# Optimization experiments

Measured on AMD Instinct MI355X. Metric: run time of the kernel, lower is better.

The kernel has to match this reference:

```python
import jax, jax.numpy as jnp
import numpy as np

# module config (mirrors init_kwargs)
D_MODEL = 1024
N_HEADS = 16
HEAD_DIM = D_MODEL // N_HEADS
WINDOW = 512
PREFIX = 16
B = 2
S = 4096  # divisible by WINDOW; S > WINDOW + PREFIX -> chunked windowed path


def setup_inputs() -> dict:
    key = jax.random.key(0)
    k1, k2, k3 = jax.random.split(key, 3)
    x = jax.random.normal(k1, (B, S, D_MODEL), dtype=jnp.float32)
    w_qkv = jax.random.normal(k2, (3 * D_MODEL, D_MODEL), dtype=jnp.float32) * 0.02
    w_out = jax.random.normal(k3, (D_MODEL, D_MODEL), dtype=jnp.float32) * 0.02
    return {"x": x, "w_qkv": w_qkv, "w_out": w_out}


def _windowed_global_attention(q, k, v):
    """q,k,v: [B,H,S,Dh]. Causal sliding-window (WINDOW) + global prefix (PREFIX) attention.
    Exactly matches torch's chunked SDPA: for query chunk starting at q_start, allowed keys are
    k_pos < PREFIX (causal) plus local keys in (q_pos-WINDOW, q_pos] with k_pos >= PREFIX."""
    Bb, H, S_, Dh = q.shape
    W, P = WINDOW, PREFIX
    C = S_ // W  # number of query chunks
    scale = 1.0 / np.sqrt(Dh).astype(np.float32)

    qc = q.reshape(Bb, H, C, W, Dh)  # [B,H,C,W,Dh]
    # pad W zero-keys at front so every chunk gathers a uniform 2W-key local tail
    kp = jnp.pad(k, ((0, 0), (0, 0), (W, 0), (0, 0)))
    vp = jnp.pad(v, ((0, 0), (0, 0), (W, 0), (0, 0)))
    tail_idx = jnp.arange(C)[:, None] * W + jnp.arange(2 * W)[None, :]  # [C,2W] (padded coords)
    kt = kp[:, :, tail_idx, :]  # [B,H,C,2W,Dh]
    vt = vp[:, :, tail_idx, :]
    kg = k[:, :, :P, :]  # global prefix keys [B,H,P,Dh]
    vg = v[:, :, :P, :]

    sg = jnp.einsum('bhcqd,bhkd->bhcqk', qc, kg) * scale   # [B,H,C,W,P]
    st = jnp.einsum('bhcqd,bhckd->bhcqk', qc, kt) * scale  # [B,H,C,W,2W]

    q_pos = jnp.arange(C)[:, None] * W + jnp.arange(W)[None, :]          # [C,W]
    kt_pos = jnp.arange(C)[:, None] * W - W + jnp.arange(2 * W)[None, :]  # [C,2W]
    # global prefix: causal only
    mg = jnp.arange(P)[None, None, :] <= q_pos[:, :, None]                # [C,W,P]
    # local tail: causal & within window & not already covered by global prefix (and not padding)
    diff = q_pos[:, :, None] - kt_pos[:, None, :]                          # [C,W,2W]
    mt = (diff >= 0) & (diff < W) & (kt_pos[:, None, :] >= P)

    neg = jnp.asarray(-1e9, sg.dtype)
    scores = jnp.concatenate([
        jnp.where(mg[None, None], sg, neg),
        jnp.where(mt[None, None], st, neg),
    ], axis=-1)  # [B,H,C,W,P+2W]
    attn = jax.nn.softmax(scores, axis=-1)

    vcat = jnp.concatenate([
        jnp.broadcast_to(vg[:, :, None], (Bb, H, C, P, Dh)), vt
    ], axis=3)  # [B,H,C,P+2W,Dh]
    out = jnp.einsum('bhcqk,bhckd->bhcqd', attn, vcat)
    return out.reshape(Bb, H, S_, Dh)


def reference(x, w_qkv, w_out):
    Bb, S_, Dm = x.shape
    qkv = x @ w_qkv.T                      # [B,S,3*Dm]
    q, k, v = jnp.split(qkv, 3, axis=-1)
    def heads(t):
        return t.reshape(Bb, S_, N_HEADS, HEAD_DIM).transpose(0, 2, 1, 3)
    q, k, v = heads(q), heads(k), heads(v)  # [B,H,S,Dh]
    o = _windowed_global_attention(q, k, v)
    o = o.transpose(0, 2, 1, 3).reshape(Bb, S_, Dm)
    return o @ w_out.T
```

## Files before the change

### kernel.cpp

```cpp
#include <hip/hip_runtime.h>
#include <hip/hip_bf16.h>

#define AS1 __attribute__((address_space(1)))
#define AS3 __attribute__((address_space(3)))

typedef unsigned short u16;
typedef short bf16x8 __attribute__((ext_vector_type(8)));
typedef unsigned short u16x8 __attribute__((ext_vector_type(8)));
typedef float f32x4 __attribute__((ext_vector_type(4)));

#define MFMA16 __builtin_amdgcn_mfma_f32_16x16x32_bf16


__device__ __forceinline__ u16 f2bf(float f) {
  union { float f; unsigned u; } c; c.f = f;
  unsigned u = c.u;
  u = u + 0x7fffu + ((u >> 16) & 1u);
  return (u16)(u >> 16);
}

__device__ __forceinline__ float fexp2(float x) {
#if __has_builtin(__builtin_amdgcn_exp2f)
  return __builtin_amdgcn_exp2f(x);
#else
  return exp2f(x);
#endif
}

__device__ __forceinline__ unsigned pack_bf(float a, float b) {
  union { float f; unsigned u; } ua, ub; ua.f = a; ub.f = b;
  return __builtin_amdgcn_perm(ub.u, ua.u, 0x07060302u);
}

__device__ __forceinline__ void gl_lds16(const void* g, void* l) {
  __builtin_amdgcn_global_load_lds((const AS1 void*)g, (AS3 void*)l, 16, 0, 0);
}


__global__ void cast_all_kernel(const float* __restrict__ x,
                                const float* __restrict__ wqkv,
                                const float* __restrict__ wout,
                                u16* __restrict__ ws) {
  int i = blockIdx.x * blockDim.x + threadIdx.x;
  const float4* src;
  int rel;
  size_t matbase;
  if (i < 2097152)      { src = (const float4*)x + i;                rel = i;           matbase = 0; }
  else if (i < 2883584) { src = (const float4*)wqkv + (i - 2097152); rel = i - 2097152; matbase = 8388608; }
  else                  { src = (const float4*)wout + (i - 2883584); rel = i - 2883584; matbase = 11534336; }
  float4 f = *src;
  ushort4 o;
  o.x = f2bf(f.x); o.y = f2bf(f.y); o.z = f2bf(f.z); o.w = f2bf(f.w);
  int fe  = rel * 4;
  int row = fe >> 10, c = fe & 1023;
  int newc = (c & ~63) | (((((c >> 3) ^ row) & 7) << 3)) | (c & 7);
  ((ushort4*)ws)[(matbase + (size_t)row * 1024 + newc) >> 2] = o;
}


template<int EPI>
__global__ __launch_bounds__(256) void gemm_bt(
    const u16* __restrict__ A, const u16* __restrict__ Bm,
    float* __restrict__ Cf,
    u16* __restrict__ qd, u16* __restrict__ kd, u16* __restrict__ vd,
    int M, int N, int K)
{
  __shared__ u16 As[128 * 64];
  __shared__ u16 Bs[128 * 64];

  const int tid  = threadIdx.x;
  const int wave = tid >> 6, lane = tid & 63;
  const int quad = lane >> 4, l16 = lane & 15;
  const int bm = blockIdx.y * 128, bn = blockIdx.x * 128;
  const int wm = (wave >> 1) * 64, wn = (wave & 1) * 64;

  f32x4 acc[4][4] = {};

  const int srow = wave * 32 + (lane >> 3);
  const int scol = (lane & 7) * 8;

  for (int kt = 0; kt < K; kt += 64) {
    __syncthreads();
    #pragma unroll
    for (int i = 0; i < 4; ++i) {
      gl_lds16(&A[(size_t)(bm + srow + i * 8) * K + kt + scol], &As[(wave * 32 + i * 8) * 64]);
      gl_lds16(&Bm[(size_t)(bn + srow + i * 8) * K + kt + scol], &Bs[(wave * 32 + i * 8) * 64]);
    }
    __syncthreads();
    #pragma unroll
    for (int kk = 0; kk < 64; kk += 32) {
      bf16x8 af[4], bb[4];
      #pragma unroll
      for (int i = 0; i < 4; ++i) {
        int row = wm + i * 16 + l16;
        af[i] = *(const bf16x8*)&As[row * 64 + (((((kk >> 3) + quad) ^ row) & 7) << 3)];
      }
      #pragma unroll
      for (int j = 0; j < 4; ++j) {
        int row = wn + j * 16 + l16;
        bb[j] = *(const bf16x8*)&Bs[row * 64 + (((((kk >> 3) + quad) ^ row) & 7) << 3)];
      }
      #pragma unroll
      for (int i = 0; i < 4; ++i)
        #pragma unroll
        for (int j = 0; j < 4; ++j)
          acc[i][j] = MFMA16(af[i], bb[j], acc[i][j], 0, 0, 0);
    }
  }

  #pragma unroll
  for (int i = 0; i < 4; ++i) {
    #pragma unroll
    for (int j = 0; j < 4; ++j) {
      #pragma unroll
      for (int r = 0; r < 4; ++r) {
        int m = bm + wm + i * 16 + quad * 4 + r;
        int n = bn + wn + j * 16 + l16;
        float val = acc[i][j][r];
        if (EPI == 0) {
          Cf[(size_t)m * N + n] = val;
        } else {
          int part = n >> 10, rem = n & 1023;
          int h = rem >> 6, d = rem & 63;
          int b = m >> 12, s = m & 4095;
          if (part == 0) val *= 0.1803368801111244f;
          u16* dst = (part == 0) ? qd : (part == 1) ? kd : vd;
          dst[((size_t)((b * 16 + h) * 4096 + s)) * 64 + d] = f2bf(val);
        }
      }
    }
  }
}


__global__ __launch_bounds__(256) void pack_v(const u16* __restrict__ vb,
                                              u16* __restrict__ vt) {
  __shared__ u16 Lt[64 * 72];
  const int tid = threadIdx.x, bid = blockIdx.x;
  const int bh = bid & 31, t = bid >> 5;
  const size_t base = (size_t)bh << 18;
  #pragma unroll
  for (int c = 0; c < 2; ++c) {
    int idx = tid * 8 + c * 2048;
    int row = idx >> 6, col = idx & 63;
    u16x8 vv = *(const u16x8*)&vb[base + (size_t)(t * 64 + row) * 64 + col];
    #pragma unroll
    for (int s = 0; s < 8; ++s) Lt[(col + s) * 72 + row] = vv[s];
  }
  __syncthreads();
  #pragma unroll
  for (int c = 0; c < 2; ++c) {
    int w = tid + c * 256;
    int dh = w >> 3, k8 = w & 7;
    u16x8 o;
    #pragma unroll
    for (int s = 0; s < 8; ++s) o[s] = Lt[dh * 72 + k8 * 8 + s];
    int off = ((dh >> 4) << 10) | ((k8 >> 2) << 9) | ((k8 & 3) << 7) | ((dh & 15) << 3);
    *(u16x8*)&vt[base + (size_t)t * 4096 + off] = o;
  }
}


__global__ __launch_bounds__(256) void attn_kernel(
    const u16* __restrict__ qb, const u16* __restrict__ kb,
    const u16* __restrict__ vt, u16* __restrict__ ob)
{
  __shared__ u16 Ps[4][32 * 64];

  const int tid  = threadIdx.x;
  const int wave = tid >> 6;
  const int lane = tid & 63;
  const int quad = lane >> 4, l16 = lane & 15;
  const int bid  = blockIdx.x;
  const int bh   = bid & 31;
  const int t0   = (((bid >> 5) << 2) | wave) << 5;
  const size_t base = (size_t)bh << 18;
  u16* __restrict__ ps = &Ps[wave][0];

  const int l64 = l16 * 64 + quad * 8;
  const u16* vbase = vt + base + lane * 8;

  const u16* qp = qb + base + (size_t)t0 * 64 + l64;
  bf16x8 bq00 = *(const bf16x8*)(qp);
  bf16x8 bq01 = *(const bf16x8*)(qp + 32);
  bf16x8 bq10 = *(const bf16x8*)(qp + 1024);
  bf16x8 bq11 = *(const bf16x8*)(qp + 1056);

  f32x4 oacc[2][4] = {};
  f32x4 lacc[2] = {};
  bf16x8 ones;
  #pragma unroll
  for (int s = 0; s < 8; ++s) ones[s] = (short)0x3F80;

  const int lo = max(0, t0 - 511) >> 6;
  const int hi = (t0 + 31) >> 6;

  auto loadK = [&](int kb0, bf16x8 (&kf)[4][2]) {
    #pragma unroll
    for (int j = 0; j < 4; ++j) {
      const u16* krow = kb + base + (size_t)(kb0 + j * 16) * 64 + l64;
      kf[j][0] = *(const bf16x8*)(krow);
      kf[j][1] = *(const bf16x8*)(krow + 32);
    }
  };

  bf16x8 ka[4][2], kb2[4][2];

  {
    const u16* kpre = kb + base + l64;
    bf16x8 pk0 = *(const bf16x8*)(kpre);
    bf16x8 pk1 = *(const bf16x8*)(kpre + 32);
    loadK(lo << 6, ka);
    bf16x8 pv[4];
    #pragma unroll
    for (int jd = 0; jd < 4; ++jd)
      pv[jd] = *(const bf16x8*)(vbase + jd * 1024);

    #pragma unroll
    for (int i = 0; i < 2; ++i) {
      f32x4 t4 = {};
      t4 = MFMA16(pk0, i ? bq10 : bq00, t4, 0, 0, 0);
      t4 = MFMA16(pk1, i ? bq11 : bq01, t4, 0, 0, 0);
      int row = i * 16 + l16;
      int qpos = t0 + row;
      float p[4];
      #pragma unroll
      for (int r = 0; r < 4; ++r) {
        int kpos = quad * 4 + r;
        p[r] = (kpos <= qpos) ? fexp2(t4[r]) : 0.f;
      }
      uint2 w;
      w.x = pack_bf(p[0], p[1]);
      w.y = pack_bf(p[2], p[3]);
      *(uint2*)&ps[row * 64 + ((quad ^ l16) & 15) * 4] = w;
      uint2 z; z.x = 0u; z.y = 0u;
      *(uint2*)&ps[row * 64 + (((4 + quad) ^ l16) & 15) * 4] = z;
    }
    #pragma unroll
    for (int i = 0; i < 2; ++i) {
      int row = i * 16 + l16;
      uint2 r0 = *(uint2*)&ps[row * 64 + (((2 * quad) ^ l16) & 15) * 4];
      uint2 r1 = *(uint2*)&ps[row * 64 + (((2 * quad + 1) ^ l16) & 15) * 4];
      union { uint4 u; bf16x8 v; } cc; cc.u = make_uint4(r0.x, r0.y, r1.x, r1.y);
      bf16x8 ap = cc.v;
      lacc[i] = MFMA16(ap, ones, lacc[i], 0, 0, 0);
      #pragma unroll
      for (int jd = 0; jd < 4; ++jd)
        oacc[i][jd] = MFMA16(ap, pv[jd], oacc[i][jd], 0, 0, 0);
    }
  }

  auto tilec = [&](int kb0, bf16x8 (&kf)[4][2]) {
    #pragma unroll
    for (int j = 0; j < 4; ++j) {
      const int kmin = kb0 + j * 16;
      #pragma unroll
      for (int i = 0; i < 2; ++i) {
        const int qmin = t0 + i * 16;
        const int row  = i * 16 + l16;
        uint2* dst = (uint2*)&ps[row * 64 + (((j * 4 + quad) ^ l16) & 15) * 4];
        const bool sub_masked = (kmin > qmin + 15) || (qmin - kmin >= 527) || (kmin < 16);
        if (sub_masked) { uint2 z; z.x = 0u; z.y = 0u; *dst = z; continue; }
        f32x4 t4 = {};
        t4 = MFMA16(kf[j][0], i ? bq10 : bq00, t4, 0, 0, 0);
        t4 = MFMA16(kf[j][1], i ? bq11 : bq01, t4, 0, 0, 0);
        const bool sub_ok = (kmin + 15 <= qmin) && (qmin + 15 - kmin < 512);
        float p[4];
        if (sub_ok) {
          #pragma unroll
          for (int r = 0; r < 4; ++r) p[r] = fexp2(t4[r]);
        } else {
          int qpos = t0 + row;
          #pragma unroll
          for (int r = 0; r < 4; ++r) {
            int kpos = kmin + quad * 4 + r;
            unsigned diff = (unsigned)(qpos - kpos);
            p[r] = (diff < 512u) ? fexp2(t4[r]) : 0.f;
          }
        }
        uint2 w;
        w.x = pack_bf(p[0], p[1]);
        w.y = pack_bf(p[2], p[3]);
        *dst = w;
      }
    }
    const u16* vp = vbase + (size_t)kb0 * 64;
    #pragma unroll
    for (int h = 0; h < 2; ++h) {
      bf16x8 bv0 = *(const bf16x8*)(vp + h * 512);
      bf16x8 bv1 = *(const bf16x8*)(vp + 1024 + h * 512);
      bf16x8 bv2 = *(const bf16x8*)(vp + 2048 + h * 512);
      bf16x8 bv3 = *(const bf16x8*)(vp + 3072 + h * 512);
      #pragma unroll
      for (int i = 0; i < 2; ++i) {
        int row = i * 16 + l16;
        int g0 = h * 8 + 2 * quad;
        uint2 r0 = *(uint2*)&ps[row * 64 + ((g0 ^ l16) & 15) * 4];
        uint2 r1 = *(uint2*)&ps[row * 64 + (((g0 + 1) ^ l16) & 15) * 4];
        union { uint4 u; bf16x8 v; } cc; cc.u = make_uint4(r0.x, r0.y, r1.x, r1.y);
        bf16x8 ap = cc.v;
        lacc[i] = MFMA16(ap, ones, lacc[i], 0, 0, 0);
        oacc[i][0] = MFMA16(ap, bv0, oacc[i][0], 0, 0, 0);
        oacc[i][1] = MFMA16(ap, bv1, oacc[i][1], 0, 0, 0);
        oacc[i][2] = MFMA16(ap, bv2, oacc[i][2], 0, 0, 0);
        oacc[i][3] = MFMA16(ap, bv3, oacc[i][3], 0, 0, 0);
      }
    }
  };

  for (int t = lo; t <= hi; t += 2) {
    if (t + 1 <= hi) loadK((t + 1) << 6, kb2);
    tilec(t << 6, ka);
    if (t + 1 <= hi) {
      if (t + 2 <= hi) loadK((t + 2) << 6, ka);
      tilec((t + 1) << 6, kb2);
    }
  }

  const int b = bh >> 4, h = bh & 15;
  #pragma unroll
  for (int i = 0; i < 2; ++i) {
    #pragma unroll
    for (int r = 0; r < 4; ++r) {
      float inv = 1.f / lacc[i][r];
      int srow = t0 + i * 16 + quad * 4 + r;
      size_t rowoff = ((size_t)(b * 4096 + srow)) * 1024 + h * 64;
      #pragma unroll
      for (int jd = 0; jd < 4; ++jd) {
        int g = ((jd * 2 + (l16 >> 3)) ^ srow) & 7;
        ob[rowoff + (g << 3) + (l16 & 7)] = f2bf(oacc[i][jd][r] * inv);
      }
    }
  }
}


extern "C" void kernel_launch(void* const* d_in, const int* in_sizes, int n_in,
                              void* d_out, int out_size, void* d_ws, size_t ws_size,
                              hipStream_t stream) {
  const float* x    = (const float*)d_in[0];
  const float* wqkv = (const float*)d_in[1];
  const float* wout = (const float*)d_in[2];
  float* out = (float*)d_out;

  u16* ws    = (u16*)d_ws;
  u16* xb    = ws;
  u16* wqkvb = xb + (size_t)8192 * 1024;
  u16* woutb = wqkvb + (size_t)3072 * 1024;
  u16* qbuf  = woutb + (size_t)1024 * 1024;
  u16* kbuf  = qbuf + (size_t)8388608;
  u16* vbuf  = kbuf + (size_t)8388608;
  u16* vtb   = vbuf + (size_t)8388608;
  u16* obuf  = xb;

  cast_all_kernel<<<12288, 256, 0, stream>>>(x, wqkv, wout, ws);

  gemm_bt<1><<<dim3(24, 64), 256, 0, stream>>>(xb, wqkvb, nullptr, qbuf, kbuf, vbuf,
                                               8192, 3072, 1024);
  pack_v<<<2048, 256, 0, stream>>>(vbuf, vtb);
  attn_kernel<<<1024, 256, 0, stream>>>(qbuf, kbuf, vtb, obuf);
  gemm_bt<0><<<dim3(8, 64), 256, 0, stream>>>(obuf, woutb, out, nullptr, nullptr, nullptr,
                                              8192, 1024, 1024);
}
```

Measured before the change: 241.4 us.

## Rewrite GEMM with 256x128 tiles, double-buffered LDS, and interleaved MFMA scheduling

```diff
diff --git a/kernel.cpp b/kernel.cpp
--- a/kernel.cpp
+++ b/kernel.cpp
@@ -10,6 +10,10 @@
 typedef float f32x4 __attribute__((ext_vector_type(4)));
 
 #define MFMA16 __builtin_amdgcn_mfma_f32_16x16x32_bf16
+
+#define SBAR()  asm volatile("s_barrier" ::: "memory")
+#define WAITV(N) asm volatile("s_waitcnt vmcnt(" #N ")" ::: "memory")
+#define WAITL0() asm volatile("s_waitcnt lgkmcnt(0)" ::: "memory")
 
 
 __device__ __forceinline__ u16 f2bf(float f) {
@@ -59,73 +63,148 @@
 
 
 template<int EPI>
-__global__ __launch_bounds__(256) void gemm_bt(
+__global__ __launch_bounds__(512, 2) void gemm_bt2(
     const u16* __restrict__ A, const u16* __restrict__ Bm,
     float* __restrict__ Cf,
     u16* __restrict__ qd, u16* __restrict__ kd, u16* __restrict__ vd,
     int M, int N, int K)
 {
-  __shared__ u16 As[128 * 64];
-  __shared__ u16 Bs[128 * 64];
+  __shared__ u16 As[2][2][128 * 64];
+  __shared__ u16 Bs[2][128 * 64];
 
   const int tid  = threadIdx.x;
   const int wave = tid >> 6, lane = tid & 63;
   const int quad = lane >> 4, l16 = lane & 15;
-  const int bm = blockIdx.y * 128, bn = blockIdx.x * 128;
-  const int wm = (wave >> 1) * 64, wn = (wave & 1) * 64;
-
-  f32x4 acc[4][4] = {};
-
-  const int srow = wave * 32 + (lane >> 3);
-  const int scol = (lane & 7) * 8;
-
-  for (int kt = 0; kt < K; kt += 64) {
-    __syncthreads();
-    #pragma unroll
-    for (int i = 0; i < 4; ++i) {
-      gl_lds16(&A[(size_t)(bm + srow + i * 8) * K + kt + scol], &As[(wave * 32 + i * 8) * 64]);
-      gl_lds16(&Bm[(size_t)(bn + srow + i * 8) * K + kt + scol], &Bs[(wave * 32 + i * 8) * 64]);
-    }
-    __syncthreads();
-    #pragma unroll
-    for (int kk = 0; kk < 64; kk += 32) {
-      bf16x8 af[4], bb[4];
-      #pragma unroll
-      for (int i = 0; i < 4; ++i) {
-        int row = wm + i * 16 + l16;
-        af[i] = *(const bf16x8*)&As[row * 64 + (((((kk >> 3) + quad) ^ row) & 7) << 3)];
-      }
-      #pragma unroll
-      for (int j = 0; j < 4; ++j) {
-        int row = wn + j * 16 + l16;
-        bb[j] = *(const bf16x8*)&Bs[row * 64 + (((((kk >> 3) + quad) ^ row) & 7) << 3)];
-      }
-      #pragma unroll
-      for (int i = 0; i < 4; ++i)
-        #pragma unroll
-        for (int j = 0; j < 4; ++j)
-          acc[i][j] = MFMA16(af[i], bb[j], acc[i][j], 0, 0, 0);
-    }
-  }
-
-  #pragma unroll
-  for (int i = 0; i < 4; ++i) {
-    #pragma unroll
-    for (int j = 0; j < 4; ++j) {
+
+  const int gx  = gridDim.x;
+  const int nwg = gx * gridDim.y;
+  const int lin = blockIdx.y * gx + blockIdx.x;
+  const int q8  = nwg >> 3;
+  const int swz = (lin & 7) * q8 + (lin >> 3);
+  const int bm = (swz / gx) * 256;
+  const int bn = (swz % gx) * 128;
+
+  const int hA = wave >> 2;
+  const int wn = (wave & 3) * 32;
+
+  const int srow = tid >> 3;
+  const int scol = (tid & 7) * 8;
+  const u16* Ab = A  + (size_t)(bm + srow) * K + scol;
+  const u16* Bb = Bm + (size_t)(bn + srow) * K + scol;
+  const int ldsw = wave * 512;
+
+  const int NT = K >> 6;
+
+  auto stA = [&](int t, int h) {
+    int d = t & 1;
+    #pragma unroll
+    for (int i = 0; i < 2; ++i)
+      gl_lds16(Ab + (size_t)(128 * h + 64 * i) * K + t * 64,
+               &As[d][h][ldsw + i * 4096]);
+  };
+  auto stB = [&](int t) {
+    int d = t & 1;
+    #pragma unroll
+    for (int i = 0; i < 2; ++i)
+      gl_lds16(Bb + (size_t)(64 * i) * K + t * 64,
+               &Bs[d][ldsw + i * 4096]);
+  };
+  auto rdA = [&](int d, int mf, int g) -> bf16x8 {
+    int row = mf * 16 + l16;
+    return *(const bf16x8*)&As[d][hA][row * 64 + (((g ^ row) & 7) << 3)];
+  };
+  auto rdB = [&](int d, int nf, int g) -> bf16x8 {
+    int row = wn + nf * 16 + l16;
+    return *(const bf16x8*)&Bs[d][row * 64 + (((g ^ row) & 7) << 3)];
+  };
+
+  f32x4 acc[8][2] = {};
+  bf16x8 fa0[8], fb0[2];
+  bf16x8 fa1[8], fb1[2];
+
+  stA(0, 0); stA(0, 1); stB(0);
+  stA(1, 0); stA(1, 1); stB(1);
+  WAITV(6);
+  SBAR();
+  #pragma unroll
+  for (int mf = 0; mf < 8; ++mf) fa0[mf] = rdA(0, mf, quad);
+  fb0[0] = rdB(0, 0, quad); fb0[1] = rdB(0, 1, quad);
+
+  for (int kt = 0; kt < NT; ++kt) {
+    const int dd = kt & 1;
+
+    #pragma unroll
+    for (int mf = 0; mf < 8; ++mf) fa1[mf] = rdA(dd, mf, quad + 4);
+    fb1[0] = rdB(dd, 0, quad + 4); fb1[1] = rdB(dd, 1, quad + 4);
+    __builtin_amdgcn_s_setprio(1);
+    #pragma unroll
+    for (int mf = 0; mf < 4; ++mf) {
+      acc[mf][0] = MFMA16(fa0[mf], fb0[0], acc[mf][0], 0, 0, 0);
+      acc[mf][1] = MFMA16(fa0[mf], fb0[1], acc[mf][1], 0, 0, 0);
+    }
+    __builtin_amdgcn_s_setprio(0);
+    SBAR();
+
+    __builtin_amdgcn_s_setprio(1);
+    #pragma unroll
+    for (int mf = 4; mf < 8; ++mf) {
+      acc[mf][0] = MFMA16(fa0[mf], fb0[0], acc[mf][0], 0, 0, 0);
+      acc[mf][1] = MFMA16(fa0[mf], fb0[1], acc[mf][1], 0, 0, 0);
+    }
+    __builtin_amdgcn_s_setprio(0);
+    WAITL0();
+    __builtin_amdgcn_sched_barrier(0);
+    SBAR();
+
+    if (kt + 2 < NT) { stA(kt + 2, 0); stB(kt + 2); }
+    __builtin_amdgcn_s_setprio(1);
+    #pragma unroll
+    for (int mf = 0; mf < 4; ++mf) {
+      acc[mf][0] = MFMA16(fa1[mf], fb1[0], acc[mf][0], 0, 0, 0);
+      acc[mf][1] = MFMA16(fa1[mf], fb1[1], acc[mf][1], 0, 0, 0);
+    }
+    __builtin_amdgcn_s_setprio(0);
+    if (kt + 1 < NT) {
+      if (kt + 2 < NT) { WAITV(4); }
+      else             { WAITV(0); }
+    }
+    SBAR();
+
+    if (kt + 2 < NT) stA(kt + 2, 1);
+    if (kt + 1 < NT) {
+      const int dn = (kt + 1) & 1;
+      #pragma unroll
+      for (int mf = 0; mf < 8; ++mf) fa0[mf] = rdA(dn, mf, quad);
+      fb0[0] = rdB(dn, 0, quad); fb0[1] = rdB(dn, 1, quad);
+    }
+    __builtin_amdgcn_s_setprio(1);
+    #pragma unroll
+    for (int mf = 4; mf < 8; ++mf) {
+      acc[mf][0] = MFMA16(fa1[mf], fb1[0], acc[mf][0], 0, 0, 0);
+      acc[mf][1] = MFMA16(fa1[mf], fb1[1], acc[mf][1], 0, 0, 0);
+    }
+    __builtin_amdgcn_s_setprio(0);
+    SBAR();
+  }
+
+  #pragma unroll
+  for (int mf = 0; mf < 8; ++mf) {
+    #pragma unroll
+    for (int nf = 0; nf < 2; ++nf) {
       #pragma unroll
       for (int r = 0; r < 4; ++r) {
-        int m = bm + wm + i * 16 + quad * 4 + r;
-        int n = bn + wn + j * 16 + l16;
-        float val = acc[i][j][r];
+        int m = bm + hA * 128 + mf * 16 + quad * 4 + r;
+        int n = bn + wn + nf * 16 + l16;
+        float val = acc[mf][nf][r];
         if (EPI == 0) {
           Cf[(size_t)m * N + n] = val;
         } else {
           int part = n >> 10, rem = n & 1023;
-          int h = rem >> 6, d = rem & 63;
+          int h = rem >> 6, dcol = rem & 63;
           int b = m >> 12, s = m & 4095;
           if (part == 0) val *= 0.1803368801111244f;
           u16* dst = (part == 0) ? qd : (part == 1) ? kd : vd;
-          dst[((size_t)((b * 16 + h) * 4096 + s)) * 64 + d] = f2bf(val);
+          dst[((size_t)((b * 16 + h) * 4096 + s)) * 64 + dcol] = f2bf(val);
         }
       }
     }
@@ -355,10 +434,10 @@
 
   cast_all_kernel<<<12288, 256, 0, stream>>>(x, wqkv, wout, ws);
 
-  gemm_bt<1><<<dim3(24, 64), 256, 0, stream>>>(xb, wqkvb, nullptr, qbuf, kbuf, vbuf,
-                                               8192, 3072, 1024);
+  gemm_bt2<1><<<dim3(24, 32), 512, 0, stream>>>(xb, wqkvb, nullptr, qbuf, kbuf, vbuf,
+                                                8192, 3072, 1024);
   pack_v<<<2048, 256, 0, stream>>>(vbuf, vtb);
   attn_kernel<<<1024, 256, 0, stream>>>(qbuf, kbuf, vtb, obuf);
-  gemm_bt<0><<<dim3(8, 64), 256, 0, stream>>>(obuf, woutb, out, nullptr, nullptr, nullptr,
-                                              8192, 1024, 1024);
-}
+  gemm_bt2<0><<<dim3(8, 32), 512, 0, stream>>>(obuf, woutb, out, nullptr, nullptr, nullptr,
+                                               8192, 1024, 1024);
+}
```

Measured after the change: 259.3 us. 7.4% more time.

## Add 256x256 double-buffered QKV GEMM with staged loads and workgroup swizzle

Applied to the files above, without the earlier changes.

```diff
diff --git a/kernel.cpp b/kernel.cpp
--- a/kernel.cpp
+++ b/kernel.cpp
@@ -10,6 +10,10 @@
 typedef float f32x4 __attribute__((ext_vector_type(4)));
 
 #define MFMA16 __builtin_amdgcn_mfma_f32_16x16x32_bf16
+
+#define SBAR()  asm volatile("s_barrier" ::: "memory")
+#define WAITV(N) asm volatile("s_waitcnt vmcnt(" #N ")" ::: "memory")
+#define WAITL0() asm volatile("s_waitcnt lgkmcnt(0)" ::: "memory")
 
 
 __device__ __forceinline__ u16 f2bf(float f) {
@@ -55,6 +59,165 @@
   int row = fe >> 10, c = fe & 1023;
   int newc = (c & ~63) | (((((c >> 3) ^ row) & 7) << 3)) | (c & 7);
   ((ushort4*)ws)[(matbase + (size_t)row * 1024 + newc) >> 2] = o;
+}
+
+
+__global__ __launch_bounds__(512, 2) void gemm_qkv(
+    const u16* __restrict__ A, const u16* __restrict__ Bm,
+    u16* __restrict__ qd, u16* __restrict__ kd, u16* __restrict__ vd,
+    int M, int N, int K)
+{
+  __shared__ u16 As[2][256 * 64];
+  __shared__ u16 Bs[2][256 * 64];
+
+  const int tid  = threadIdx.x;
+  const int wave = tid >> 6, lane = tid & 63;
+  const int quad = lane >> 4, l16 = lane & 15;
+  const int wr = wave >> 2, wc = wave & 3;
+
+  const int gx  = gridDim.x;
+  const int nwg = gx * gridDim.y;
+  const int lin = blockIdx.y * gx + blockIdx.x;
+  const int q8  = nwg >> 3;
+  const int swz = (lin & 7) * q8 + (lin >> 3);
+  const int bm = (swz / gx) * 256;
+  const int bn = (swz % gx) * 256;
+
+  const int sr = lane >> 3;
+  const int sc = (lane & 7) * 8;
+  const u16* Abase = A  + (size_t)(bm + wave * 8 + sr) * K + sc;
+  const u16* Bbase = Bm + (size_t)(bn + sr) * K + sc;
+  const int w4 = (wave >> 2) * 64 + (wave & 3) * 8;
+
+  const int NT = K >> 6;
+
+  auto stA = [&](int t, int h) {
+    const int d = t & 1;
+    #pragma unroll
+    for (int c = 0; c < 2; ++c) {
+      int rb = h * 64 + c * 128;
+      gl_lds16(Abase + (size_t)rb * K + (size_t)t * 64,
+               &As[d][(rb + wave * 8) * 64]);
+    }
+  };
+  auto stB = [&](int t, int h) {
+    const int d = t & 1;
+    #pragma unroll
+    for (int c = 0; c < 2; ++c) {
+      int rb = w4 + h * 32 + c * 128;
+      gl_lds16(Bbase + (size_t)rb * K + (size_t)t * 64,
+               &Bs[d][rb * 64]);
+    }
+  };
+  auto rdA = [&](int d, int mf, int g) -> bf16x8 {
+    int row = wr * 128 + mf * 16 + l16;
+    return *(const bf16x8*)&As[d][row * 64 + (((g ^ row) & 7) << 3)];
+  };
+  auto rdB = [&](int d, int nf, int g) -> bf16x8 {
+    int row = wc * 64 + nf * 16 + l16;
+    return *(const bf16x8*)&Bs[d][row * 64 + (((g ^ row) & 7) << 3)];
+  };
+
+  f32x4 acc[8][4] = {};
+  bf16x8 aA[4][2];
+  bf16x8 bB[4][2];
+
+  stA(0, 0); stB(0, 0); stB(0, 1); stA(0, 1);
+  stA(1, 0); stB(1, 0); stB(1, 1);
+  WAITV(6);
+  SBAR();
+
+  for (int X = 0; X < NT; ++X) {
+    const int d  = X & 1;
+    const bool s1 = (X + 1 < NT);
+    const bool s2 = (X + 2 < NT);
+
+    #pragma unroll
+    for (int mf = 0; mf < 4; ++mf) { aA[mf][0] = rdA(d, mf, quad); aA[mf][1] = rdA(d, mf, quad + 4); }
+    #pragma unroll
+    for (int nf = 0; nf < 2; ++nf) { bB[nf][0] = rdB(d, nf, quad); bB[nf][1] = rdB(d, nf, quad + 4); }
+    if (s1) stA(X + 1, 1);
+    SBAR();
+    WAITL0();
+    __builtin_amdgcn_s_setprio(1);
+    #pragma unroll
+    for (int mf = 0; mf < 4; ++mf)
+      #pragma unroll
+      for (int nf = 0; nf < 2; ++nf) {
+        acc[mf][nf] = MFMA16(aA[mf][0], bB[nf][0], acc[mf][nf], 0, 0, 0);
+        acc[mf][nf] = MFMA16(aA[mf][1], bB[nf][1], acc[mf][nf], 0, 0, 0);
+      }
+    __builtin_amdgcn_s_setprio(0);
+    SBAR();
+
+    #pragma unroll
+    for (int nf = 2; nf < 4; ++nf) { bB[nf][0] = rdB(d, nf, quad); bB[nf][1] = rdB(d, nf, quad + 4); }
+    if (s2) stA(X + 2, 0);
+    SBAR();
+    WAITL0();
+    __builtin_amdgcn_s_setprio(1);
+    #pragma unroll
+    for (int mf = 0; mf < 4; ++mf)
+      #pragma unroll
+      for (int nf = 2; nf < 4; ++nf) {
+        acc[mf][nf] = MFMA16(aA[mf][0], bB[nf][0], acc[mf][nf], 0, 0, 0);
+        acc[mf][nf] = MFMA16(aA[mf][1], bB[nf][1], acc[mf][nf], 0, 0, 0);
+      }
+    __builtin_amdgcn_s_setprio(0);
+    SBAR();
+
+    #pragma unroll
+    for (int mf = 0; mf < 4; ++mf) { aA[mf][0] = rdA(d, mf + 4, quad); aA[mf][1] = rdA(d, mf + 4, quad + 4); }
+    if (s2) stB(X + 2, 0);
+    SBAR();
+    WAITL0();
+    __builtin_amdgcn_s_setprio(1);
+    #pragma unroll
+    for (int mf = 0; mf < 4; ++mf)
+      #pragma unroll
+      for (int nf = 0; nf < 2; ++nf) {
+        acc[mf + 4][nf] = MFMA16(aA[mf][0], bB[nf][0], acc[mf + 4][nf], 0, 0, 0);
+        acc[mf + 4][nf] = MFMA16(aA[mf][1], bB[nf][1], acc[mf + 4][nf], 0, 0, 0);
+      }
+    __builtin_amdgcn_s_setprio(0);
+    SBAR();
+
+    if (s2) stB(X + 2, 1);
+    SBAR();
+    __builtin_amdgcn_s_setprio(1);
+    #pragma unroll
+    for (int mf = 0; mf < 4; ++mf)
+      #pragma unroll
+      for (int nf = 2; nf < 4; ++nf) {
+        acc[mf + 4][nf] = MFMA16(aA[mf][0], bB[nf][0], acc[mf + 4][nf], 0, 0, 0);
+        acc[mf + 4][nf] = MFMA16(aA[mf][1], bB[nf][1], acc[mf + 4][nf], 0, 0, 0);
+      }
+    __builtin_amdgcn_s_setprio(0);
+    if (s1) {
+      if (s2) { WAITV(6); }
+      else    { WAITV(0); }
+    }
+    SBAR();
+  }
+
+  #pragma unroll
+  for (int mf = 0; mf < 8; ++mf) {
+    #pragma unroll
+    for (int nf = 0; nf < 4; ++nf) {
+      #pragma unroll
+      for (int r = 0; r < 4; ++r) {
+        int m = bm + wr * 128 + mf * 16 + quad * 4 + r;
+        int n = bn + wc * 64 + nf * 16 + l16;
+        float val = acc[mf][nf][r];
+        int part = n >> 10, rem = n & 1023;
+        int h = rem >> 6, dcol = rem & 63;
+        int b = m >> 12, s = m & 4095;
+        if (part == 0) val *= 0.1803368801111244f;
+        u16* dst = (part == 0) ? qd : (part == 1) ? kd : vd;
+        dst[((size_t)((b * 16 + h) * 4096 + s)) * 64 + dcol] = f2bf(val);
+      }
+    }
+  }
 }
 
 
@@ -355,8 +518,8 @@
 
   cast_all_kernel<<<12288, 256, 0, stream>>>(x, wqkv, wout, ws);
 
-  gemm_bt<1><<<dim3(24, 64), 256, 0, stream>>>(xb, wqkvb, nullptr, qbuf, kbuf, vbuf,
-                                               8192, 3072, 1024);
+  gemm_qkv<<<dim3(12, 32), 512, 0, stream>>>(xb, wqkvb, qbuf, kbuf, vbuf,
+                                             8192, 3072, 1024);
   pack_v<<<2048, 256, 0, stream>>>(vbuf, vtb);
   attn_kernel<<<1024, 256, 0, stream>>>(qbuf, kbuf, vtb, obuf);
   gemm_bt<0><<<dim3(8, 64), 256, 0, stream>>>(obuf, woutb, out, nullptr, nullptr, nullptr,
```

New measurement: 245.3 us. No clear change (+1.6%).

## Fuse V transpose-pack into QKV GEMM epilogue and raise MFMA wave priority

Applied to the files above, without the earlier changes.

```diff
diff --git a/kernel.cpp b/kernel.cpp
--- a/kernel.cpp
+++ b/kernel.cpp
@@ -108,55 +108,49 @@
     }
   }
 
-  #pragma unroll
-  for (int i = 0; i < 4; ++i) {
-    #pragma unroll
-    for (int j = 0; j < 4; ++j) {
-      #pragma unroll
-      for (int r = 0; r < 4; ++r) {
-        int m = bm + wm + i * 16 + quad * 4 + r;
-        int n = bn + wn + j * 16 + l16;
-        float val = acc[i][j][r];
-        if (EPI == 0) {
-          Cf[(size_t)m * N + n] = val;
-        } else {
-          int part = n >> 10, rem = n & 1023;
-          int h = rem >> 6, d = rem & 63;
-          int b = m >> 12, s = m & 4095;
-          if (part == 0) val *= 0.1803368801111244f;
-          u16* dst = (part == 0) ? qd : (part == 1) ? kd : vd;
-          dst[((size_t)((b * 16 + h) * 4096 + s)) * 64 + d] = f2bf(val);
+  const int partU = bn >> 10;
+  if (EPI == 1 && partU == 2) {
+    const int b = bm >> 12;
+    #pragma unroll
+    for (int i = 0; i < 4; ++i) {
+      int s0q = (bm + wm + i * 16 + quad * 4) & 4095;
+      int t  = s0q >> 6, k6 = s0q & 63;
+      int h2 = k6 >> 5, q2 = (k6 >> 3) & 3, ssb = k6 & 7;
+      #pragma unroll
+      for (int j = 0; j < 4; ++j) {
+        int nbase = bn + wn + j * 16;
+        int h  = (nbase >> 6) & 15;
+        int jd = (nbase & 63) >> 4;
+        unsigned lo = (unsigned)f2bf(acc[i][j][0]) | ((unsigned)f2bf(acc[i][j][1]) << 16);
+        unsigned hi = (unsigned)f2bf(acc[i][j][2]) | ((unsigned)f2bf(acc[i][j][3]) << 16);
+        uint2 w; w.x = lo; w.y = hi;
+        *(uint2*)&vd[(((size_t)(b * 16 + h)) << 18) + (size_t)t * 4096
+                     + jd * 1024 + h2 * 512 + (q2 * 16 + l16) * 8 + ssb] = w;
+      }
+    }
+  } else {
+    #pragma unroll
+    for (int i = 0; i < 4; ++i) {
+      #pragma unroll
+      for (int j = 0; j < 4; ++j) {
+        #pragma unroll
+        for (int r = 0; r < 4; ++r) {
+          int m = bm + wm + i * 16 + quad * 4 + r;
+          int n = bn + wn + j * 16 + l16;
+          float val = acc[i][j][r];
+          if (EPI == 0) {
+            Cf[(size_t)m * N + n] = val;
+          } else {
+            int part = n >> 10, rem = n & 1023;
+            int h = rem >> 6, d = rem & 63;
+            int b = m >> 12, s = m & 4095;
+            if (part == 0) val *= 0.1803368801111244f;
+            u16* dst = (part == 0) ? qd : kd;
+            dst[((size_t)((b * 16 + h) * 4096 + s)) * 64 + d] = f2bf(val);
+          }
         }
       }
     }
-  }
-}
-
-
-__global__ __launch_bounds__(256) void pack_v(const u16* __restrict__ vb,
-                                              u16* __restrict__ vt) {
-  __shared__ u16 Lt[64 * 72];
-  const int tid = threadIdx.x, bid = blockIdx.x;
-  const int bh = bid & 31, t = bid >> 5;
-  const size_t base = (size_t)bh << 18;
-  #pragma unroll
-  for (int c = 0; c < 2; ++c) {
-    int idx = tid * 8 + c * 2048;
-    int row = idx >> 6, col = idx & 63;
-    u16x8 vv = *(const u16x8*)&vb[base + (size_t)(t * 64 + row) * 64 + col];
-    #pragma unroll
-    for (int s = 0; s < 8; ++s) Lt[(col + s) * 72 + row] = vv[s];
-  }
-  __syncthreads();
-  #pragma unroll
-  for (int c = 0; c < 2; ++c) {
-    int w = tid + c * 256;
-    int dh = w >> 3, k8 = w & 7;
-    u16x8 o;
-    #pragma unroll
-    for (int s = 0; s < 8; ++s) o[s] = Lt[dh * 72 + k8 * 8 + s];
-    int off = ((dh >> 4) << 10) | ((k8 >> 2) << 9) | ((k8 & 3) << 7) | ((dh & 15) << 3);
-    *(u16x8*)&vt[base + (size_t)t * 4096 + off] = o;
   }
 }
 
@@ -243,10 +237,12 @@
       uint2 r1 = *(uint2*)&ps[row * 64 + (((2 * quad + 1) ^ l16) & 15) * 4];
       union { uint4 u; bf16x8 v; } cc; cc.u = make_uint4(r0.x, r0.y, r1.x, r1.y);
       bf16x8 ap = cc.v;
+      __builtin_amdgcn_s_setprio(1);
       lacc[i] = MFMA16(ap, ones, lacc[i], 0, 0, 0);
       #pragma unroll
       for (int jd = 0; jd < 4; ++jd)
         oacc[i][jd] = MFMA16(ap, pv[jd], oacc[i][jd], 0, 0, 0);
+      __builtin_amdgcn_s_setprio(0);
     }
   }
 
@@ -262,8 +258,10 @@
         const bool sub_masked = (kmin > qmin + 15) || (qmin - kmin >= 527) || (kmin < 16);
         if (sub_masked) { uint2 z; z.x = 0u; z.y = 0u; *dst = z; continue; }
         f32x4 t4 = {};
+        __builtin_amdgcn_s_setprio(1);
         t4 = MFMA16(kf[j][0], i ? bq10 : bq00, t4, 0, 0, 0);
         t4 = MFMA16(kf[j][1], i ? bq11 : bq01, t4, 0, 0, 0);
+        __builtin_amdgcn_s_setprio(0);
         const bool sub_ok = (kmin + 15 <= qmin) && (qmin + 15 - kmin < 512);
         float p[4];
         if (sub_ok) {
@@ -299,11 +297,13 @@
         uint2 r1 = *(uint2*)&ps[row * 64 + (((g0 + 1) ^ l16) & 15) * 4];
         union { uint4 u; bf16x8 v; } cc; cc.u = make_uint4(r0.x, r0.y, r1.x, r1.y);
         bf16x8 ap = cc.v;
+        __builtin_amdgcn_s_setprio(1);
         lacc[i] = MFMA16(ap, ones, lacc[i], 0, 0, 0);
         oacc[i][0] = MFMA16(ap, bv0, oacc[i][0], 0, 0, 0);
         oacc[i][1] = MFMA16(ap, bv1, oacc[i][1], 0, 0, 0);
         oacc[i][2] = MFMA16(ap, bv2, oacc[i][2], 0, 0, 0);
         oacc[i][3] = MFMA16(ap, bv3, oacc[i][3], 0, 0, 0);
+        __builtin_amdgcn_s_setprio(0);
       }
     }
   };
@@ -355,9 +355,8 @@
 
   cast_all_kernel<<<12288, 256, 0, stream>>>(x, wqkv, wout, ws);
 
-  gemm_bt<1><<<dim3(24, 64), 256, 0, stream>>>(xb, wqkvb, nullptr, qbuf, kbuf, vbuf,
+  gemm_bt<1><<<dim3(24, 64), 256, 0, stream>>>(xb, wqkvb, nullptr, qbuf, kbuf, vtb,
                                                8192, 3072, 1024);
-  pack_v<<<2048, 256, 0, stream>>>(vbuf, vtb);
   attn_kernel<<<1024, 256, 0, stream>>>(qbuf, kbuf, vtb, obuf);
   gemm_bt<0><<<dim3(8, 64), 256, 0, stream>>>(obuf, woutb, out, nullptr, nullptr, nullptr,
                                               8192, 1024, 1024);
```

Result: faster. 233.2 us (-3.4%).
